# Optimization experiments

Hardware: AMD Instinct MI355X
Metric: run time of the kernel (lower is better)

## Reference

```python
import jax, jax.numpy as jnp
import numpy as np

B, D, K, U = 4096, 1024, 5, 1024  # batch, input_dim, num_basis, units


def setup_inputs() -> dict:
    key = jax.random.key(0)
    k1, k2, k3 = jax.random.split(key, 3)
    x = jax.random.normal(k1, (B, D), dtype=jnp.float32)
    basis_weights = jax.random.normal(k2, (D, K, U), dtype=jnp.float32) * 0.02
    bias = jax.random.normal(k3, (U,), dtype=jnp.float32) * 0.02
    return {"x": x, "basis_weights": basis_weights, "bias": bias}


def reference(x, basis_weights, bias):
    # Polynomial basis expansion: x^0, x^1, ..., x^{K-1}  -> (B, D, K)
    num_basis = basis_weights.shape[1]
    powers = jnp.arange(num_basis, dtype=x.dtype)
    basis = x[..., None] ** powers  # x**0 == 1, matching tf.ones_like branch
    # Fused: einsum('bik,ikj->bij') followed by reduce_sum over i == 'bik,ikj->bj'.
    # Avoids materializing the (B, D, U) intermediate of the original.
    out = jnp.einsum("bik,ikj->bj", basis, basis_weights) + bias
    # tf.nn.gelu defaults to exact (non-approximate) GELU.
    return jax.nn.gelu(out, approximate=False)
```

## Files before the change

### kernel.cpp

```cpp
#include <hip/hip_runtime.h>
#include <hip/hip_bf16.h>
#include <math.h>


#define B_DIM 4096
#define D_DIM 1024
#define U_DIM 1024
#define NKB 128

typedef unsigned short ushort_t;
typedef __attribute__((ext_vector_type(8))) short bf16x8;
typedef __attribute__((ext_vector_type(4))) float f32x4;
typedef __attribute__((ext_vector_type(2))) float f32x2;

__device__ __forceinline__ ushort_t f2bf(float f) {
  union { float f; unsigned int u; } v;
  v.f = f;
  unsigned int r = v.u + 0x7FFFu + ((v.u >> 16) & 1u);
  return (ushort_t)(r >> 16);
}

__device__ __forceinline__ void load_lds16(const ushort_t* g, ushort_t* l) {
  __builtin_amdgcn_global_load_lds(
      (const __attribute__((address_space(1))) ushort_t*)g,
      (__attribute__((address_space(3))) ushort_t*)l, 16, 0, 0);
}

__device__ __forceinline__ float gelu_exact(float v) {
  return 0.5f * v * (1.0f + erff(v * 0.70710678118654752f));
}

__global__ __launch_bounds__(256) void w_pack_kernel(
    const float* __restrict__ W, ushort_t* __restrict__ Bp,
    float* __restrict__ fold32) {
  __shared__ float red[64];
  const int bidx = blockIdx.x;
  const int n16  = bidx >> 5;
  const int kq   = bidx & 31;
  const int wave = threadIdx.x >> 6;
  const int lane = threadIdx.x & 63;
  const int m    = lane & 15;
  const int ko   = lane >> 4;
  const int j    = n16 * 16 + m;
  const int kblk = kq * 4 + wave;
  const int i0   = kblk * 8 + ko * 2;

  ushort_t o[8];
  float s0 = 0.0f;
#pragma unroll
  for (int t2 = 0; t2 < 2; ++t2) {
    const int i = i0 + t2;
    s0 += W[(size_t)(i * 5) * U_DIM + j];
#pragma unroll
    for (int e = 0; e < 4; ++e)
      o[t2 * 4 + e] = f2bf(W[(size_t)(i * 5 + e + 1) * U_DIM + j]);
  }
  *(uint4*)(Bp + ((size_t)n16 * NKB + kblk) * 512 + lane * 8) = *(const uint4*)o;

  s0 += __shfl_xor(s0, 16, 64);
  s0 += __shfl_xor(s0, 32, 64);
  if (ko == 0) red[wave * 16 + m] = s0;
  __syncthreads();
  if (wave == 0 && ko == 0)
    fold32[(size_t)j * 32 + kq] =
        red[m] + red[16 + m] + red[32 + m] + red[48 + m];
}

__global__ __launch_bounds__(256) void fold_final_kernel(
    const float* __restrict__ fold32, const float* __restrict__ bias,
    float* __restrict__ b2) {
  const int j = blockIdx.x * 256 + threadIdx.x;
  const float4* fp = (const float4*)(fold32 + (size_t)j * 32);
  float s = bias[j];
#pragma unroll
  for (int g = 0; g < 8; ++g) {
    const float4 f = fp[g];
    s += f.x + f.y + f.z + f.w;
  }
  b2[j] = s;
}

__global__ __launch_bounds__(256) void gemm_kernel(
    const float* __restrict__ x, const ushort_t* __restrict__ Bp,
    const float* __restrict__ b2, float* __restrict__ C) {
  __shared__ __align__(16) ushort_t lds[4][5120];

  const int tid  = threadIdx.x;
  const int wave = tid >> 6;
  const int lane = tid & 63;
  const int wm   = wave >> 1;
  const int wn   = wave & 1;
  const int m    = lane & 15;
  const int ko   = lane >> 4;

  const int lin  = blockIdx.y * 8 + blockIdx.x;
  const int xcd  = lin & 7;
  const int slot = lin >> 3;
  const int mt   = xcd * 8 + (slot & 7);
  const int nt   = slot >> 3;
  const int m16b = mt * 4;
  const int n16b = nt * 8;

  const int xrow  = (wave & 1) * 32 + (lane >> 1);
  const int xchk  = (lane & 1) ^ ((lane >> 3) & 1);
  const ushort_t* gx =
      (const ushort_t*)(x + ((size_t)(m16b * 16 + xrow)) * D_DIM + xchk * 4);
  const int ldx = (wave & 1) * 512 + lane * 8;

  const ushort_t* gb0 = Bp + ((size_t)(n16b + wave) * NKB) * 512 + lane * 8;
  const ushort_t* gb1 = Bp + ((size_t)(n16b + 4 + wave) * NKB) * 512 + lane * 8;
  const int ldb0 = 1024 + wave * 512 + lane * 8;
  const int ldb1 = 1024 + (4 + wave) * 512 + lane * 8;

  const int xoff = wm * 1024 + m * 32 +
                   ((((ko >> 1) ^ ((m >> 2) & 1))) << 4) + (ko & 1) * 8;

  f32x4 acc[2][4];
  const f32x4 zero = {0.0f, 0.0f, 0.0f, 0.0f};
#pragma unroll
  for (int mf = 0; mf < 2; ++mf)
#pragma unroll
    for (int nf = 0; nf < 4; ++nf) acc[mf][nf] = zero;

#define WAITBAR(N) \
  asm volatile("s_waitcnt vmcnt(" #N ")\n\ts_barrier" ::: "memory")

#define STAGE_X(bb, rel)                                                \
  do {                                                                  \
    load_lds16(gx  + (rel) * 16,  &lds[bb][ldx]);                       \
    load_lds16(gb0 + (rel) * 512, &lds[bb][ldb0]);                      \
    load_lds16(gb1 + (rel) * 512, &lds[bb][ldb1]);                      \
  } while (0)

#define STAGE_Y(bb, rel)                                                \
  do {                                                                  \
    load_lds16(gb0 + (rel) * 512, &lds[bb][ldb0]);                      \
    load_lds16(gb1 + (rel) * 512, &lds[bb][ldb1]);                      \
  } while (0)

#define PACKA(dst, xp)                                                  \
  do {                                                                  \
    const f32x2 p1 = (xp);                                              \
    const f32x2 p2 = p1 * p1;                                           \
    const f32x2 p3 = p2 * p1;                                           \
    const f32x2 p4 = p2 * p2;                                           \
    union { bf16x8 v; unsigned int u[4]; } r_;                          \
    asm("v_cvt_pk_bf16_f32 %0, %1, %2" : "=v"(r_.u[0]) : "v"(p1[0]), "v"(p2[0])); \
    asm("v_cvt_pk_bf16_f32 %0, %1, %2" : "=v"(r_.u[1]) : "v"(p3[0]), "v"(p4[0])); \
    asm("v_cvt_pk_bf16_f32 %0, %1, %2" : "=v"(r_.u[2]) : "v"(p1[1]), "v"(p2[1])); \
    asm("v_cvt_pk_bf16_f32 %0, %1, %2" : "=v"(r_.u[3]) : "v"(p3[1]), "v"(p4[1])); \
    dst = r_.v;                                                         \
  } while (0)

#define COMPUTE(bb)                                                     \
  do {                                                                  \
    const char* xu = (const char*)&lds[bb][0];                          \
    const f32x2 q0 = *(const f32x2*)(xu + xoff);                        \
    const f32x2 q1 = *(const f32x2*)(xu + xoff + 512);                  \
    bf16x8 a[2], b[4];                                                  \
    PACKA(a[0], q0);                                                    \
    PACKA(a[1], q1);                                                    \
    _Pragma("unroll")                                                   \
    for (int nf = 0; nf < 4; ++nf)                                      \
      b[nf] = *(const bf16x8*)&lds[bb][1024 + (wn * 4 + nf) * 512 + lane * 8]; \
    _Pragma("unroll")                                                   \
    for (int mf = 0; mf < 2; ++mf)                                      \
      _Pragma("unroll")                                                 \
      for (int nf = 0; nf < 4; ++nf)                                    \
        acc[mf][nf] = __builtin_amdgcn_mfma_f32_16x16x32_bf16(          \
            a[mf], b[nf], acc[mf][nf], 0, 0, 0);                        \
  } while (0)

  if (wave < 2) {
    STAGE_X(0, 0);
    STAGE_X(1, 1);
    STAGE_X(2, 2);
    gx  += 4 * 16;
    gb0 += 4 * 512;
    gb1 += 4 * 512;
    for (int base = 0; base < 124; base += 4) {
      WAITBAR(6); STAGE_X(3, -1); COMPUTE(0);
      WAITBAR(6); STAGE_X(0,  0); COMPUTE(1);
      WAITBAR(6); STAGE_X(1,  1); COMPUTE(2);
      WAITBAR(6); STAGE_X(2,  2); COMPUTE(3);
      gx  += 4 * 16;
      gb0 += 4 * 512;
      gb1 += 4 * 512;
    }
    WAITBAR(6); STAGE_X(3, -1); COMPUTE(0);
    WAITBAR(6); COMPUTE(1);
    WAITBAR(3); COMPUTE(2);
    WAITBAR(0); COMPUTE(3);
  } else {
    STAGE_Y(0, 0);
    STAGE_Y(1, 1);
    STAGE_Y(2, 2);
    gb0 += 4 * 512;
    gb1 += 4 * 512;
    for (int base = 0; base < 124; base += 4) {
      WAITBAR(4); STAGE_Y(3, -1); COMPUTE(0);
      WAITBAR(4); STAGE_Y(0,  0); COMPUTE(1);
      WAITBAR(4); STAGE_Y(1,  1); COMPUTE(2);
      WAITBAR(4); STAGE_Y(2,  2); COMPUTE(3);
      gb0 += 4 * 512;
      gb1 += 4 * 512;
    }
    WAITBAR(4); STAGE_Y(3, -1); COMPUTE(0);
    WAITBAR(4); COMPUTE(1);
    WAITBAR(2); COMPUTE(2);
    WAITBAR(0); COMPUTE(3);
  }
#undef STAGE_X
#undef STAGE_Y
#undef COMPUTE
#undef PACKA
#undef WAITBAR

  const int crow0 = m16b * 16 + wm * 32 + (lane >> 4) * 4;
  const int ccol0 = n16b * 16 + wn * 64 + m;
#pragma unroll
  for (int nf = 0; nf < 4; ++nf) {
    const int col = ccol0 + nf * 16;
    const float bv = b2[col];
#pragma unroll
    for (int mf = 0; mf < 2; ++mf) {
#pragma unroll
      for (int r = 0; r < 4; ++r) {
        const int row = crow0 + mf * 16 + r;
        C[(size_t)row * U_DIM + col] = gelu_exact(acc[mf][nf][r] + bv);
      }
    }
  }
}

__global__ void fallback_kernel(const float* __restrict__ x, const float* __restrict__ W,
                                const float* __restrict__ bias, float* __restrict__ out) {
  int j  = blockIdx.x * 256 + threadIdx.x;
  int b0 = blockIdx.y * 16;
  float acc[16];
#pragma unroll
  for (int t = 0; t < 16; ++t) acc[t] = 0.0f;
  for (int i = 0; i < D_DIM; ++i) {
    const float* wr = W + (size_t)i * 5 * U_DIM + j;
    float w0 = wr[0 * U_DIM], w1 = wr[1 * U_DIM], w2 = wr[2 * U_DIM];
    float w3 = wr[3 * U_DIM], w4 = wr[4 * U_DIM];
#pragma unroll
    for (int t = 0; t < 16; ++t) {
      float xv = x[(size_t)(b0 + t) * D_DIM + i];
      float x2 = xv * xv;
      acc[t] += w0 + xv * w1 + x2 * w2 + x2 * xv * w3 + x2 * x2 * w4;
    }
  }
  float bv = bias[j];
#pragma unroll
  for (int t = 0; t < 16; ++t)
    out[(size_t)(b0 + t) * U_DIM + j] = gelu_exact(acc[t] + bv);
}

extern "C" void kernel_launch(void* const* d_in, const int* in_sizes, int n_in,
                              void* d_out, int out_size, void* d_ws, size_t ws_size,
                              hipStream_t stream) {
  const float* x    = (const float*)d_in[0];
  const float* W    = (const float*)d_in[1];
  const float* bias = (const float*)d_in[2];
  float* out = (float*)d_out;

  const size_t szB = (size_t)U_DIM * 4096 * sizeof(ushort_t);
  const size_t szF = (size_t)32 * U_DIM * sizeof(float);
  const size_t szb = (size_t)U_DIM * sizeof(float);

  if (ws_size >= szB + szF + szb) {
    ushort_t* Bp   = (ushort_t*)d_ws;
    float*    f32p = (float*)((char*)d_ws + szB);
    float*    b2   = (float*)((char*)d_ws + szB + szF);
    w_pack_kernel<<<dim3(2048), 256, 0, stream>>>(W, Bp, f32p);
    fold_final_kernel<<<dim3(U_DIM / 256), 256, 0, stream>>>(f32p, bias, b2);
    gemm_kernel<<<dim3(U_DIM / 128, B_DIM / 64), 256, 0, stream>>>(x, Bp, b2, out);
  } else {
    fallback_kernel<<<dim3(U_DIM / 256, B_DIM / 16), 256, 0, stream>>>(x, W, bias, out);
  }
}
```

Baseline: 130.6 us.

## Double-buffer LDS fragment reads in registers to overlap with MFMA

Splits the compute step into an LDS-read/pack phase and an MFMA phase, with two register fragment sets. The next stage's x values are packed to bf16 polynomial terms and its weight fragments are loaded while the MFMAs for the current stage run. The goal is to hide LDS read latency and packing ALU work behind matrix math. In exchange the barrier wait counts are tightened, which shortens the effective global-load prefetch depth, and register pressure rises from holding two fragment sets.

```diff
diff --git a/kernel.cpp b/kernel.cpp
--- a/kernel.cpp
+++ b/kernel.cpp
@@ -122,6 +122,8 @@
 #pragma unroll
     for (int nf = 0; nf < 4; ++nf) acc[mf][nf] = zero;
 
+  bf16x8 a0[2], b0[4], a1[2], b1[4];
+
 #define WAITBAR(N) \
   asm volatile("s_waitcnt vmcnt(" #N ")\n\ts_barrier" ::: "memory")
 
@@ -152,23 +154,26 @@
     dst = r_.v;                                                         \
   } while (0)
 
-#define COMPUTE(bb)                                                     \
-  do {                                                                  \
-    const char* xu = (const char*)&lds[bb][0];                          \
-    const f32x2 q0 = *(const f32x2*)(xu + xoff);                        \
-    const f32x2 q1 = *(const f32x2*)(xu + xoff + 512);                  \
-    bf16x8 a[2], b[4];                                                  \
-    PACKA(a[0], q0);                                                    \
-    PACKA(a[1], q1);                                                    \
+#define PREREAD(s, bb)                                                  \
+  do {                                                                  \
+    const char* xu_ = (const char*)&lds[bb][0];                         \
+    const f32x2 q0_ = *(const f32x2*)(xu_ + xoff);                      \
+    const f32x2 q1_ = *(const f32x2*)(xu_ + xoff + 512);                \
+    PACKA(a##s[0], q0_);                                                \
+    PACKA(a##s[1], q1_);                                                \
     _Pragma("unroll")                                                   \
     for (int nf = 0; nf < 4; ++nf)                                      \
-      b[nf] = *(const bf16x8*)&lds[bb][1024 + (wn * 4 + nf) * 512 + lane * 8]; \
+      b##s[nf] = *(const bf16x8*)&lds[bb][1024 + (wn * 4 + nf) * 512 + lane * 8]; \
+  } while (0)
+
+#define MFMA4(s)                                                        \
+  do {                                                                  \
     _Pragma("unroll")                                                   \
     for (int mf = 0; mf < 2; ++mf)                                      \
       _Pragma("unroll")                                                 \
       for (int nf = 0; nf < 4; ++nf)                                    \
         acc[mf][nf] = __builtin_amdgcn_mfma_f32_16x16x32_bf16(          \
-            a[mf], b[nf], acc[mf][nf], 0, 0, 0);                        \
+            a##s[mf], b##s[nf], acc[mf][nf], 0, 0, 0);                  \
   } while (0)
 
   if (wave < 2) {
@@ -178,41 +183,46 @@
     gx  += 4 * 16;
     gb0 += 4 * 512;
     gb1 += 4 * 512;
+    WAITBAR(6);
+    PREREAD(0, 0);
     for (int base = 0; base < 124; base += 4) {
-      WAITBAR(6); STAGE_X(3, -1); COMPUTE(0);
-      WAITBAR(6); STAGE_X(0,  0); COMPUTE(1);
-      WAITBAR(6); STAGE_X(1,  1); COMPUTE(2);
-      WAITBAR(6); STAGE_X(2,  2); COMPUTE(3);
+      WAITBAR(3); STAGE_X(3, -1); PREREAD(1, 1); MFMA4(0);
+      WAITBAR(3); STAGE_X(0,  0); PREREAD(0, 2); MFMA4(1);
+      WAITBAR(3); STAGE_X(1,  1); PREREAD(1, 3); MFMA4(0);
+      WAITBAR(3); STAGE_X(2,  2); PREREAD(0, 0); MFMA4(1);
       gx  += 4 * 16;
       gb0 += 4 * 512;
       gb1 += 4 * 512;
     }
-    WAITBAR(6); STAGE_X(3, -1); COMPUTE(0);
-    WAITBAR(6); COMPUTE(1);
-    WAITBAR(3); COMPUTE(2);
-    WAITBAR(0); COMPUTE(3);
+    WAITBAR(3); STAGE_X(3, -1); PREREAD(1, 1); MFMA4(0);
+    WAITBAR(3); PREREAD(0, 2); MFMA4(1);
+    WAITBAR(0); PREREAD(1, 3); MFMA4(0);
+    MFMA4(1);
   } else {
     STAGE_Y(0, 0);
     STAGE_Y(1, 1);
     STAGE_Y(2, 2);
     gb0 += 4 * 512;
     gb1 += 4 * 512;
+    WAITBAR(4);
+    PREREAD(0, 0);
     for (int base = 0; base < 124; base += 4) {
-      WAITBAR(4); STAGE_Y(3, -1); COMPUTE(0);
-      WAITBAR(4); STAGE_Y(0,  0); COMPUTE(1);
-      WAITBAR(4); STAGE_Y(1,  1); COMPUTE(2);
-      WAITBAR(4); STAGE_Y(2,  2); COMPUTE(3);
+      WAITBAR(2); STAGE_Y(3, -1); PREREAD(1, 1); MFMA4(0);
+      WAITBAR(2); STAGE_Y(0,  0); PREREAD(0, 2); MFMA4(1);
+      WAITBAR(2); STAGE_Y(1,  1); PREREAD(1, 3); MFMA4(0);
+      WAITBAR(2); STAGE_Y(2,  2); PREREAD(0, 0); MFMA4(1);
       gb0 += 4 * 512;
       gb1 += 4 * 512;
     }
-    WAITBAR(4); STAGE_Y(3, -1); COMPUTE(0);
-    WAITBAR(4); COMPUTE(1);
-    WAITBAR(2); COMPUTE(2);
-    WAITBAR(0); COMPUTE(3);
+    WAITBAR(2); STAGE_Y(3, -1); PREREAD(1, 1); MFMA4(0);
+    WAITBAR(2); PREREAD(0, 2); MFMA4(1);
+    WAITBAR(0); PREREAD(1, 3); MFMA4(0);
+    MFMA4(1);
   }
 #undef STAGE_X
 #undef STAGE_Y
-#undef COMPUTE
+#undef PREREAD
+#undef MFMA4
 #undef PACKA
 #undef WAITBAR
 
```

New measurement: 130.9 us. No clear change (+0.2%).
